# Kernel tuning notes

Measured on AMD Instinct MI355X. Metric: run time of the kernel, lower is better.

The kernel has to match this reference:

```python
import jax, jax.numpy as jnp
import numpy as np

C = 256
CK = C // 8  # query/key projection dim

def conv1x1(x, w, b):
    # x: (B,C,H,W), w: (O,C), b: (O,)
    return jnp.einsum('bchw,oc->bohw', x, w) + b[None, :, None, None]

def conv3x3(x, w, b):
    # w: (O,C,3,3)
    y = jax.lax.conv_general_dilated(x, w, window_strides=(1, 1), padding='SAME',
                                     dimension_numbers=('NCHW', 'OIHW', 'NCHW'))
    return y + b[None, :, None, None]

def setup_inputs() -> dict:
    key = jax.random.key(0)
    ks = jax.random.split(key, 24)
    s = 0.05
    d = {
        'x1': jax.random.normal(ks[0], (4, C, 64, 64), jnp.float32),
        'x2': jax.random.normal(ks[1], (4, C, 64, 64), jnp.float32),
        'wq1': jax.random.normal(ks[2], (CK, C), jnp.float32) * s,
        'bq1': jax.random.normal(ks[3], (CK,), jnp.float32) * s,
        'wk1': jax.random.normal(ks[4], (CK, C), jnp.float32) * s,
        'bk1': jax.random.normal(ks[5], (CK,), jnp.float32) * s,
        'wv1': jax.random.normal(ks[6], (C, C), jnp.float32) * s,
        'bv1': jax.random.normal(ks[7], (C,), jnp.float32) * s,
        'wq2': jax.random.normal(ks[8], (CK, C), jnp.float32) * s,
        'bq2': jax.random.normal(ks[9], (CK,), jnp.float32) * s,
        'wk2': jax.random.normal(ks[10], (CK, C), jnp.float32) * s,
        'bk2': jax.random.normal(ks[11], (CK,), jnp.float32) * s,
        'wv2': jax.random.normal(ks[12], (C, C), jnp.float32) * s,
        'bv2': jax.random.normal(ks[13], (C,), jnp.float32) * s,
        'wd1': jax.random.normal(ks[14], (C, C), jnp.float32) * s,
        'bd1': jax.random.normal(ks[15], (C,), jnp.float32) * s,
        'wd3': jax.random.normal(ks[16], (C, C, 3, 3), jnp.float32) * s,
        'bd3': jax.random.normal(ks[17], (C,), jnp.float32) * s,
        'gamma1': jax.random.normal(ks[18], (1,), jnp.float32) * 0.5,
        'gamma2': jax.random.normal(ks[19], (1,), jnp.float32) * 0.5,
    }
    return d

def reference(x1, x2, wq1, bq1, wk1, bk1, wv1, bv1, wq2, bq2, wk2, bk2, wv2, bv2,
              wd1, bd1, wd3, bd3, gamma1, gamma2):
    B, Cc, H, W = x1.shape
    N = H * W
    # projections (1x1 convs), flattened to (B, d, N)
    q1 = conv1x1(x1, wq1, bq1).reshape(B, CK, N)
    k1 = conv1x1(x1, wk1, bk1).reshape(B, CK, N)
    v1 = conv1x1(x1, wv1, bv1).reshape(B, Cc, N)
    q2 = conv1x1(x2, wq2, bq2).reshape(B, CK, N)
    k2 = conv1x1(x2, wk2, bk2).reshape(B, CK, N)
    v2 = conv1x1(x2, wv2, bv2).reshape(B, Cc, N)
    # cross attention 1: queries from x1, keys/values from x2
    energy1 = jnp.einsum('bdi,bdj->bij', q1, k2)          # (B,N,N)
    attn1 = jax.nn.softmax(energy1, axis=-1)
    out1 = jnp.einsum('bcj,bij->bci', v2, attn1).reshape(B, Cc, H, W)
    # cross attention 2: queries from x2, keys/values from x1
    energy2 = jnp.einsum('bdi,bdj->bij', q2, k1)
    attn2 = jax.nn.softmax(energy2, axis=-1)
    out2 = jnp.einsum('bcj,bij->bci', v1, attn2).reshape(B, Cc, H, W)
    # residual conv branches + gamma-scaled skip (norm1/norm2 in source are dead code)
    out1 = out1 + conv1x1(x1, wd1, bd1) + conv3x3(x1, wd3, bd3)
    out2 = out2 + conv1x1(x2, wd1, bd1) + conv3x3(x2, wd3, bd3)
    out1 = x1 + gamma1[0] * out1
    out2 = x2 + gamma2[0] * out2
    return (out1, out2)
```

## Files before the change

kernel.cpp:

```cpp
#include <hip/hip_runtime.h>
#include <hip/hip_bf16.h>

#define CC 256
#define CKD 32
#define NN 4096
#define HH 64
#define WW 64
#define BB 4

#define LOG2E 1.44269504088896f
#define EXPSHIFT 23.0831203874f

typedef __attribute__((ext_vector_type(8))) short short8;
typedef __attribute__((ext_vector_type(4))) float floatx4;

__device__ __forceinline__ unsigned f2bf(float f) {
  union { float f; unsigned u; } v; v.f = f;
  unsigned r = v.u + 0x7fffu + ((v.u >> 16) & 1u);
  return r >> 16;
}
__device__ __forceinline__ unsigned short f2bf_fast(float f) {
  return (unsigned short)((__float_as_uint(f) + 0x8000u) >> 16);
}
__device__ __forceinline__ float fast_exp2(float x) {
#if __has_builtin(__builtin_amdgcn_exp2f)
  return __builtin_amdgcn_exp2f(x);
#else
  return __expf(x * 0.693147181f);
#endif
}

__global__ __launch_bounds__(256) void xpack_kernel(
    const float* __restrict__ x1, const float* __restrict__ x2,
    unsigned short* __restrict__ Xp) {
  const int t = threadIdx.x;
  const int nb = blockIdx.x, cbk = blockIdx.y, img = blockIdx.z;
  const float* X = ((img >> 2) ? x2 : x1) + (size_t)(img & 3) * CC * NN;
  const int n0 = nb * 64, c0 = cbk * 64;
  __shared__ float tile[64][65];
  const int nl = t & 63, cl0 = t >> 6;
#pragma unroll
  for (int i = 0; i < 16; ++i)
    tile[cl0 + i * 4][nl] = X[(size_t)(c0 + cl0 + i * 4) * NN + n0 + nl];
  __syncthreads();
#pragma unroll
  for (int it = 0; it < 2; ++it) {
    int id = it * 256 + t;
    int nl2 = id >> 3, cc = id & 7;
    short8 v;
#pragma unroll
    for (int j = 0; j < 8; ++j) v[j] = (short)f2bf(tile[cc * 8 + j][nl2]);
    *(short8*)(Xp + (size_t)img * NN * CC + (size_t)(n0 + nl2) * CC + c0 + cc * 8) = v;
  }
}

__global__ __launch_bounds__(256) void wpack_kernel(
    const float* __restrict__ wd1, const float* __restrict__ wd3,
    const float* __restrict__ wq1, const float* __restrict__ wk1,
    const float* __restrict__ wv1,
    const float* __restrict__ wq2, const float* __restrict__ wk2,
    const float* __restrict__ wv2,
    const float* __restrict__ bq1, const float* __restrict__ bk1,
    const float* __restrict__ bv1,
    const float* __restrict__ bq2, const float* __restrict__ bk2,
    const float* __restrict__ bv2,
    unsigned short* __restrict__ Wp, unsigned short* __restrict__ Wqkv,
    float* __restrict__ Bias) {
  const int id = blockIdx.x * 256 + threadIdx.x;
#pragma unroll
  for (int tap = 0; tap < 10; ++tap) {
    float v = (tap < 9) ? wd3[(size_t)id * 9 + tap] : wd1[id];
    Wp[(size_t)tap * (CC * CC) + id] = (unsigned short)f2bf(v);
  }
#pragma unroll
  for (int j = 0; j < 3; ++j) {
    int e = id + j * 65536;
    if (e < 2 * 320 * 256) {
      int inp = e / (320 * 256), rem = e % (320 * 256);
      int o = rem >> 8, c = rem & 255;
      float v;
      if (inp == 0)
        v = (o < 32) ? wq1[o * 256 + c] * LOG2E
            : (o < 64) ? wk1[(o - 32) * 256 + c] : wv1[(o - 64) * 256 + c];
      else
        v = (o < 32) ? wq2[o * 256 + c] * LOG2E
            : (o < 64) ? wk2[(o - 32) * 256 + c] : wv2[(o - 64) * 256 + c];
      Wqkv[e] = (unsigned short)f2bf(v);
    }
  }
  if (id < 640) {
    int inp = id / 320, o = id % 320;
    float v;
    if (inp == 0) v = (o < 32) ? bq1[o] * LOG2E
                      : (o < 64) ? bk1[o - 32] : bv1[o - 64];
    else          v = (o < 32) ? bq2[o] * LOG2E
                      : (o < 64) ? bk2[o - 32] : bv2[o - 64];
    Bias[id] = v;
  }
}

__global__ __launch_bounds__(256) void proj_mfma_kernel(
    const unsigned short* __restrict__ Xp, const unsigned short* __restrict__ Wqkv,
    const float* __restrict__ Bias,
    unsigned short* __restrict__ Qp1, unsigned short* __restrict__ Kp1,
    unsigned short* __restrict__ Vp1,
    unsigned short* __restrict__ Qp2, unsigned short* __restrict__ Kp2,
    unsigned short* __restrict__ Vp2) {
  const int t = threadIdx.x;
  const int w = t >> 6, lane = t & 63;
  const int l15 = lane & 15, g = lane >> 4;
  const int img = blockIdx.x, pb = blockIdx.y;
  const int pix0 = pb * 64;
  const int inp = img >> 2, b = img & 3;
  const unsigned short* Xi = Xp + (size_t)img * NN * CC;
  const unsigned short* Wb = Wqkv + (size_t)inp * 320 * CC;
  const float* Bi = Bias + inp * 320;
  unsigned short* Qp = (inp ? Qp2 : Qp1) + (size_t)b * NN * CKD;
  unsigned short* Kp = (inp ? Kp2 : Kp1) + (size_t)b * NN * CKD;
  unsigned short* Vp = (inp ? Vp2 : Vp1) + (size_t)b * NN * CC;

  __shared__ unsigned short tile[320][72];

  floatx4 acc[4][5];
#pragma unroll
  for (int mf = 0; mf < 4; ++mf)
#pragma unroll
    for (int nf = 0; nf < 5; ++nf) acc[mf][nf] = (floatx4){0.f, 0.f, 0.f, 0.f};
  const int o0w = w * 80;

#pragma unroll
  for (int cb = 0; cb < 8; ++cb) {
    short8 a[4], bfr[5];
#pragma unroll
    for (int mf = 0; mf < 4; ++mf)
      a[mf] = *(const short8*)(Xi + (size_t)(pix0 + mf * 16 + l15) * CC + cb * 32 + g * 8);
#pragma unroll
    for (int nf = 0; nf < 5; ++nf)
      bfr[nf] = *(const short8*)(Wb + (size_t)(o0w + nf * 16 + l15) * CC + cb * 32 + g * 8);
#pragma unroll
    for (int nf = 0; nf < 5; ++nf)
#pragma unroll
      for (int mf = 0; mf < 4; ++mf)
        acc[mf][nf] = __builtin_amdgcn_mfma_f32_16x16x32_bf16(
            a[mf], bfr[nf], acc[mf][nf], 0, 0, 0);
  }

#pragma unroll
  for (int nf = 0; nf < 5; ++nf) {
    float bs = Bi[o0w + nf * 16 + l15];
#pragma unroll
    for (int mf = 0; mf < 4; ++mf) {
      uint2 pk;
      pk.x = f2bf(acc[mf][nf][0] + bs) | (f2bf(acc[mf][nf][1] + bs) << 16);
      pk.y = f2bf(acc[mf][nf][2] + bs) | (f2bf(acc[mf][nf][3] + bs) << 16);
      *(uint2*)&tile[o0w + nf * 16 + l15][mf * 16 + g * 4] = pk;
    }
  }
  __syncthreads();

  {
    const int pix = t >> 2, ch = t & 3;
    short8 vq, vk;
#pragma unroll
    for (int e = 0; e < 8; ++e) {
      vq[e] = (short)tile[ch * 8 + e][pix];
      vk[e] = (short)tile[32 + ch * 8 + e][pix];
    }
    *(short8*)(Qp + (size_t)(pix0 + pix) * CKD + ch * 8) = vq;
    *(short8*)(Kp + (size_t)(pix0 + pix) * CKD + ch * 8) = vk;
  }
#pragma unroll
  for (int it = 0; it < 8; ++it) {
    short8 vv = *(const short8*)&tile[64 + t][it * 8];
    *(short8*)(Vp + ((size_t)((pix0 >> 3) + it) * CC + t) * 8) = vv;
  }
}

__global__ __launch_bounds__(256, 2) void conv_mfma_kernel(
    const unsigned short* __restrict__ Xp, const unsigned short* __restrict__ Wp,
    const float* __restrict__ bd1, const float* __restrict__ bd3,
    unsigned short* __restrict__ R1, unsigned short* __restrict__ R2) {
  const int t = threadIdx.x;
  const int w = t >> 6, lane = t & 63;
  const int l15 = lane & 15, g = lane >> 4;
  const int ob = blockIdx.x, img = blockIdx.y, pb = blockIdx.z;
  const int o0 = ob * 128, n0 = pb * 128, y0 = pb * 2;
  const int wm = w >> 1, wn = w & 1;

  const unsigned short* Xi = Xp + (size_t)img * NN * CC;
  unsigned short* R = ((img >> 2) ? R2 : R1) + (size_t)(img & 3) * CC * NN;

  __shared__ unsigned short xs[4][66][72];

  floatx4 acc[4][4];
#pragma unroll
  for (int m = 0; m < 4; ++m)
#pragma unroll
    for (int n = 0; n < 4; ++n) acc[m][n] = (floatx4){0.f, 0.f, 0.f, 0.f};

  for (int cb = 0; cb < 4; ++cb) {
    const int c0 = cb * 64;
    __syncthreads();
#pragma unroll
    for (int it = 0; it < 9; ++it) {
      int id = it * 256 + t;
      if (id < 2112) {
        int r = id / 528, rem = id % 528;
        int col = rem >> 3, cc = rem & 7;
        int y = y0 - 1 + r, x = col - 1;
        short8 v = {0, 0, 0, 0, 0, 0, 0, 0};
        if (y >= 0 && y < HH && x >= 0 && x < WW)
          v = *(const short8*)(Xi + (size_t)(y * WW + x) * CC + c0 + cc * 8);
        *(short8*)&xs[r][col][cc * 8] = v;
      }
    }
    __syncthreads();
#pragma unroll
    for (int tap = 0; tap < 10; ++tap) {
      const int dy = (tap < 9) ? tap / 3 - 1 : 0;
      const int dx = (tap < 9) ? tap % 3 - 1 : 0;
      const int rrow = 1 + wn + dy;
      const unsigned short* wrow =
          Wp + (size_t)(tap * CC + o0 + wm * 64 + l15) * CC + c0 + g * 8;
#pragma unroll
      for (int ks = 0; ks < 2; ++ks) {
        short8 af[4], bf[4];
#pragma unroll
        for (int m = 0; m < 4; ++m)
          af[m] = *(const short8*)(wrow + (size_t)(m * 16) * CC + ks * 32);
#pragma unroll
        for (int n = 0; n < 4; ++n)
          bf[n] = *(const short8*)&xs[rrow][1 + n * 16 + l15 + dx][ks * 32 + g * 8];
#pragma unroll
        for (int m = 0; m < 4; ++m)
#pragma unroll
          for (int n = 0; n < 4; ++n)
            acc[m][n] = __builtin_amdgcn_mfma_f32_16x16x32_bf16(
                af[m], bf[n], acc[m][n], 0, 0, 0);
      }
    }
  }

#pragma unroll
  for (int m = 0; m < 4; ++m) {
    int ob2 = o0 + wm * 64 + m * 16 + g * 4;
    float bs[4];
#pragma unroll
    for (int r = 0; r < 4; ++r) bs[r] = bd1[ob2 + r] + bd3[ob2 + r];
#pragma unroll
    for (int n = 0; n < 4; ++n) {
      int pix = n0 + wn * 64 + n * 16 + l15;
#pragma unroll
      for (int r = 0; r < 4; ++r)
        R[(size_t)(ob2 + r) * NN + pix] = f2bf_fast(acc[m][n][r] + bs[r]);
    }
  }
}

__global__ __launch_bounds__(256, 2) void attn_kernel(
    const unsigned short* __restrict__ Qp1, const unsigned short* __restrict__ Kp1,
    const unsigned short* __restrict__ Qp2, const unsigned short* __restrict__ Kp2,
    const unsigned short* __restrict__ Vp1, const unsigned short* __restrict__ Vp2,
    const unsigned short* __restrict__ R1, const unsigned short* __restrict__ R2,
    const float* __restrict__ x1, const float* __restrict__ x2,
    const float* __restrict__ g1, const float* __restrict__ g2,
    float* __restrict__ out) {
  const int t = threadIdx.x;
  const int w = t >> 6, lane = t & 63;
  const int l15 = lane & 15, g = lane >> 4;
  const int att = blockIdx.x, b = blockIdx.y;
  const int i0 = blockIdx.z * 64;

  const unsigned short *Qp, *Kp, *Vp, *Rb; const float *x; float gamma; float* o;
  if (att == 0) { Qp = Qp1; Kp = Kp2; Vp = Vp2; Rb = R1; x = x1; gamma = g1[0]; o = out; }
  else          { Qp = Qp2; Kp = Kp1; Vp = Vp1; Rb = R2; x = x2; gamma = g2[0];
                  o = out + (size_t)BB * CC * NN; }
  Qp += (size_t)b * NN * CKD; Kp += (size_t)b * NN * CKD; Vp += (size_t)b * NN * CC;
  Rb += (size_t)b * CC * NN; x += (size_t)b * CC * NN; o += (size_t)b * CC * NN;

  __shared__ unsigned short p_s[2][64][72];
  __shared__ float l_s[64];

  short8 bq = *(const short8*)(Qp + (size_t)(i0 + w * 16 + l15) * CKD + g * 8);

  floatx4 acc[4][4];
#pragma unroll
  for (int a = 0; a < 4; ++a)
#pragma unroll
    for (int c = 0; c < 4; ++c) acc[a][c] = (floatx4){0.f, 0.f, 0.f, 0.f};
  float l_acc = 0.f;
  const floatx4 zinit = {-EXPSHIFT, -EXPSHIFT, -EXPSHIFT, -EXPSHIFT};

  short8 kr[2][4], vr[2][8];
#pragma unroll
  for (int js = 0; js < 4; ++js)
    kr[0][js] = *(const short8*)(Kp + (size_t)(js * 16 + l15) * CKD + g * 8);
#pragma unroll
  for (int ks = 0; ks < 2; ++ks)
#pragma unroll
    for (int cs = 0; cs < 4; ++cs)
      vr[0][ks * 4 + cs] = *(const short8*)(Vp +
          ((size_t)(ks * 4 + g) * CC + (w * 64 + cs * 16 + l15)) * 8);

#pragma unroll 2
  for (int jt = 0; jt < NN / 64; ++jt) {
    const int cur = jt & 1, nxt = cur ^ 1;
    if (jt + 1 < NN / 64) {
      const size_t j0n = (size_t)(jt + 1) * 64;
#pragma unroll
      for (int js = 0; js < 4; ++js)
        kr[nxt][js] = *(const short8*)(Kp + (j0n + js * 16 + l15) * CKD + g * 8);
#pragma unroll
      for (int ks = 0; ks < 2; ++ks)
#pragma unroll
        for (int cs = 0; cs < 4; ++cs)
          vr[nxt][ks * 4 + cs] = *(const short8*)(Vp +
              (((j0n >> 3) + ks * 4 + g) * CC + (w * 64 + cs * 16 + l15)) * 8);
    }
#pragma unroll
    for (int js = 0; js < 4; ++js) {
      floatx4 s = __builtin_amdgcn_mfma_f32_16x16x32_bf16(kr[cur][js], bq, zinit, 0, 0, 0);
      float p0 = fast_exp2(s[0]);
      float p1 = fast_exp2(s[1]);
      float p2 = fast_exp2(s[2]);
      float p3 = fast_exp2(s[3]);
      l_acc += (p0 + p1) + (p2 + p3);
      unsigned u0 = __float_as_uint(p0) + 0x8000u;
      unsigned u1 = __float_as_uint(p1) + 0x8000u;
      unsigned u2 = __float_as_uint(p2) + 0x8000u;
      unsigned u3 = __float_as_uint(p3) + 0x8000u;
      uint2 pk;
      pk.x = __builtin_amdgcn_perm(u1, u0, 0x07060302u);
      pk.y = __builtin_amdgcn_perm(u3, u2, 0x07060302u);
      *(uint2*)&p_s[cur][w * 16 + l15][js * 16 + g * 4] = pk;
    }
    __syncthreads();
#pragma unroll
    for (int ks = 0; ks < 2; ++ks) {
      short8 ap[4];
#pragma unroll
      for (int isub = 0; isub < 4; ++isub)
        ap[isub] = *(const short8*)&p_s[cur][isub * 16 + l15][ks * 32 + g * 8];
#pragma unroll
      for (int cs = 0; cs < 4; ++cs)
#pragma unroll
        for (int isub = 0; isub < 4; ++isub)
          acc[isub][cs] = __builtin_amdgcn_mfma_f32_16x16x32_bf16(
              ap[isub], vr[cur][ks * 4 + cs], acc[isub][cs], 0, 0, 0);
    }
  }

  l_acc += __shfl_xor(l_acc, 16);
  l_acc += __shfl_xor(l_acc, 32);
  if (g == 0) l_s[w * 16 + l15] = l_acc;
  __syncthreads();

#pragma unroll
  for (int isub = 0; isub < 4; ++isub) {
    float linv[4];
#pragma unroll
    for (int r = 0; r < 4; ++r) linv[r] = 1.f / l_s[isub * 16 + g * 4 + r];
#pragma unroll
    for (int cs = 0; cs < 4; ++cs) {
      int c = w * 64 + cs * 16 + l15;
      size_t base = (size_t)c * NN + i0 + isub * 16 + g * 4;
      float4 xr = *(const float4*)(x + base);
      uint2 rr = *(const uint2*)(Rb + base);
      float r0 = __uint_as_float(rr.x << 16);
      float r1 = __uint_as_float(rr.x & 0xffff0000u);
      float r2 = __uint_as_float(rr.y << 16);
      float r3 = __uint_as_float(rr.y & 0xffff0000u);
      float4 ov;
      ov.x = xr.x + gamma * (acc[isub][cs][0] * linv[0] + r0);
      ov.y = xr.y + gamma * (acc[isub][cs][1] * linv[1] + r1);
      ov.z = xr.z + gamma * (acc[isub][cs][2] * linv[2] + r2);
      ov.w = xr.w + gamma * (acc[isub][cs][3] * linv[3] + r3);
      *(float4*)(o + base) = ov;
    }
  }
}

extern "C" void kernel_launch(void* const* d_in, const int* in_sizes, int n_in,
                              void* d_out, int out_size, void* d_ws, size_t ws_size,
                              hipStream_t stream) {
  const float* x1  = (const float*)d_in[0];
  const float* x2  = (const float*)d_in[1];
  const float* wq1 = (const float*)d_in[2];
  const float* bq1 = (const float*)d_in[3];
  const float* wk1 = (const float*)d_in[4];
  const float* bk1 = (const float*)d_in[5];
  const float* wv1 = (const float*)d_in[6];
  const float* bv1 = (const float*)d_in[7];
  const float* wq2 = (const float*)d_in[8];
  const float* bq2 = (const float*)d_in[9];
  const float* wk2 = (const float*)d_in[10];
  const float* bk2 = (const float*)d_in[11];
  const float* wv2 = (const float*)d_in[12];
  const float* bv2 = (const float*)d_in[13];
  const float* wd1 = (const float*)d_in[14];
  const float* bd1 = (const float*)d_in[15];
  const float* wd3 = (const float*)d_in[16];
  const float* bd3 = (const float*)d_in[17];
  const float* g1  = (const float*)d_in[18];
  const float* g2  = (const float*)d_in[19];
  float* out = (float*)d_out;

  const size_t QB = (size_t)BB * NN * CKD * 2;
  const size_t VB = (size_t)BB * NN * CC * 2;
  const size_t RB = (size_t)BB * NN * CC * 2;
  const size_t XB = (size_t)2 * BB * NN * CC * 2;
  const size_t WPB = (size_t)10 * CC * CC * 2;
  const size_t WQB = (size_t)2 * 320 * CC * 2;
  char* base = (char*)d_ws;
  unsigned short* R1 = (unsigned short*)(base);
  unsigned short* R2 = (unsigned short*)(base + RB);
  unsigned short* Qp1 = (unsigned short*)(base + 2 * RB);
  unsigned short* Kp1 = (unsigned short*)(base + 2 * RB + QB);
  unsigned short* Qp2 = (unsigned short*)(base + 2 * RB + 2 * QB);
  unsigned short* Kp2 = (unsigned short*)(base + 2 * RB + 3 * QB);
  unsigned short* Vp1 = (unsigned short*)(base + 2 * RB + 4 * QB);
  unsigned short* Vp2 = (unsigned short*)(base + 2 * RB + 4 * QB + VB);
  unsigned short* Xp  = (unsigned short*)(base + 2 * RB + 4 * QB + 2 * VB);
  unsigned short* Wp  = (unsigned short*)(base + 2 * RB + 4 * QB + 2 * VB + XB);
  unsigned short* Wqkv = (unsigned short*)(base + 2 * RB + 4 * QB + 2 * VB + XB + WPB);
  float* Bias = (float*)(base + 2 * RB + 4 * QB + 2 * VB + XB + WPB + WQB);

  xpack_kernel<<<dim3(NN / 64, CC / 64, 2 * BB), 256, 0, stream>>>(x1, x2, Xp);
  wpack_kernel<<<dim3(CC * CC / 256), 256, 0, stream>>>(
      wd1, wd3, wq1, wk1, wv1, wq2, wk2, wv2,
      bq1, bk1, bv1, bq2, bk2, bv2, Wp, Wqkv, Bias);

  proj_mfma_kernel<<<dim3(2 * BB, NN / 64), 256, 0, stream>>>(
      Xp, Wqkv, Bias, Qp1, Kp1, Vp1, Qp2, Kp2, Vp2);

  conv_mfma_kernel<<<dim3(2, 2 * BB, NN / 128), 256, 0, stream>>>(
      Xp, Wp, bd1, bd3, R1, R2);

  attn_kernel<<<dim3(2, BB, NN / 64), 256, 0, stream>>>(
      Qp1, Kp1, Qp2, Kp2, Vp1, Vp2, R1, R2, x1, x2, g1, g2, out);
}
```

Measured before the change: 316.9 us.

## Fuse input packing into projection, widen conv and attention blocks to 512 threads

The separate xpack kernel is removed. The projection kernel now loads fp32 x, converts it to bf16 in shared memory, writes the packed copy for the conv kernel, and runs its MFMAs from LDS. The conv kernel uses 512 threads over 4 image rows per block. The attention kernel uses 512 threads (8 waves) that split the key tiles and channels, with partial row sums reduced through shared memory and a software-pipelined K/V prefetch across ping-pong P buffers. The aim is to cut one launch and one global round trip and to raise occupancy, at the cost of more registers per wave and more synchronisation.

```diff
diff --git a/kernel.cpp b/kernel.cpp
--- a/kernel.cpp
+++ b/kernel.cpp
@@ -19,8 +19,8 @@
   unsigned r = v.u + 0x7fffu + ((v.u >> 16) & 1u);
   return r >> 16;
 }
-__device__ __forceinline__ unsigned short f2bf_fast(float f) {
-  return (unsigned short)((__float_as_uint(f) + 0x8000u) >> 16);
+__device__ __forceinline__ unsigned f2bf_fast(float f) {
+  return (__float_as_uint(f) + 0x8000u) >> 16;
 }
 __device__ __forceinline__ float fast_exp2(float x) {
 #if __has_builtin(__builtin_amdgcn_exp2f)
@@ -29,30 +29,8 @@
   return __expf(x * 0.693147181f);
 #endif
 }
-
-__global__ __launch_bounds__(256) void xpack_kernel(
-    const float* __restrict__ x1, const float* __restrict__ x2,
-    unsigned short* __restrict__ Xp) {
-  const int t = threadIdx.x;
-  const int nb = blockIdx.x, cbk = blockIdx.y, img = blockIdx.z;
-  const float* X = ((img >> 2) ? x2 : x1) + (size_t)(img & 3) * CC * NN;
-  const int n0 = nb * 64, c0 = cbk * 64;
-  __shared__ float tile[64][65];
-  const int nl = t & 63, cl0 = t >> 6;
-#pragma unroll
-  for (int i = 0; i < 16; ++i)
-    tile[cl0 + i * 4][nl] = X[(size_t)(c0 + cl0 + i * 4) * NN + n0 + nl];
-  __syncthreads();
-#pragma unroll
-  for (int it = 0; it < 2; ++it) {
-    int id = it * 256 + t;
-    int nl2 = id >> 3, cc = id & 7;
-    short8 v;
-#pragma unroll
-    for (int j = 0; j < 8; ++j) v[j] = (short)f2bf(tile[cc * 8 + j][nl2]);
-    *(short8*)(Xp + (size_t)img * NN * CC + (size_t)(n0 + nl2) * CC + c0 + cc * 8) = v;
-  }
-}
+__device__ __forceinline__ float bf_lo(unsigned u) { return __uint_as_float(u << 16); }
+__device__ __forceinline__ float bf_hi(unsigned u) { return __uint_as_float(u & 0xffff0000u); }
 
 __global__ __launch_bounds__(256) void wpack_kernel(
     const float* __restrict__ wd1, const float* __restrict__ wd3,
@@ -99,9 +77,10 @@
   }
 }
 
-__global__ __launch_bounds__(256) void proj_mfma_kernel(
-    const unsigned short* __restrict__ Xp, const unsigned short* __restrict__ Wqkv,
-    const float* __restrict__ Bias,
+__global__ __launch_bounds__(256) void proj_kernel(
+    const float* __restrict__ x1, const float* __restrict__ x2,
+    const unsigned short* __restrict__ Wqkv, const float* __restrict__ Bias,
+    unsigned short* __restrict__ Xp,
     unsigned short* __restrict__ Qp1, unsigned short* __restrict__ Kp1,
     unsigned short* __restrict__ Vp1,
     unsigned short* __restrict__ Qp2, unsigned short* __restrict__ Kp2,
@@ -112,14 +91,40 @@
   const int img = blockIdx.x, pb = blockIdx.y;
   const int pix0 = pb * 64;
   const int inp = img >> 2, b = img & 3;
-  const unsigned short* Xi = Xp + (size_t)img * NN * CC;
+  const float* X = (inp ? x2 : x1) + (size_t)b * CC * NN;
   const unsigned short* Wb = Wqkv + (size_t)inp * 320 * CC;
   const float* Bi = Bias + inp * 320;
   unsigned short* Qp = (inp ? Qp2 : Qp1) + (size_t)b * NN * CKD;
   unsigned short* Kp = (inp ? Kp2 : Kp1) + (size_t)b * NN * CKD;
   unsigned short* Vp = (inp ? Vp2 : Vp1) + (size_t)b * NN * CC;
-
-  __shared__ unsigned short tile[320][72];
+  unsigned short* Xo = Xp + (size_t)img * NN * CC;
+
+  __shared__ union {
+    float ftile[64][65];
+    unsigned short otile[320][72];
+  } pu;
+  __shared__ unsigned short xt[64][264];
+
+  const int nl = t & 63, cl0 = t >> 6;
+  for (int cb = 0; cb < 4; ++cb) {
+    const int c0 = cb * 64;
+    if (cb) __syncthreads();
+#pragma unroll
+    for (int i = 0; i < 16; ++i)
+      pu.ftile[cl0 + i * 4][nl] = X[(size_t)(c0 + cl0 + i * 4) * NN + pix0 + nl];
+    __syncthreads();
+#pragma unroll
+    for (int it = 0; it < 2; ++it) {
+      int id = it * 256 + t;
+      int p = id >> 3, cc = id & 7;
+      short8 v;
+#pragma unroll
+      for (int j = 0; j < 8; ++j) v[j] = (short)f2bf(pu.ftile[cc * 8 + j][p]);
+      *(short8*)&xt[p][c0 + cc * 8] = v;
+      *(short8*)(Xo + (size_t)(pix0 + p) * CC + c0 + cc * 8) = v;
+    }
+  }
+  __syncthreads();
 
   floatx4 acc[4][5];
 #pragma unroll
@@ -133,7 +138,7 @@
     short8 a[4], bfr[5];
 #pragma unroll
     for (int mf = 0; mf < 4; ++mf)
-      a[mf] = *(const short8*)(Xi + (size_t)(pix0 + mf * 16 + l15) * CC + cb * 32 + g * 8);
+      a[mf] = *(const short8*)&xt[mf * 16 + l15][cb * 32 + g * 8];
 #pragma unroll
     for (int nf = 0; nf < 5; ++nf)
       bfr[nf] = *(const short8*)(Wb + (size_t)(o0w + nf * 16 + l15) * CC + cb * 32 + g * 8);
@@ -153,7 +158,7 @@
       uint2 pk;
       pk.x = f2bf(acc[mf][nf][0] + bs) | (f2bf(acc[mf][nf][1] + bs) << 16);
       pk.y = f2bf(acc[mf][nf][2] + bs) | (f2bf(acc[mf][nf][3] + bs) << 16);
-      *(uint2*)&tile[o0w + nf * 16 + l15][mf * 16 + g * 4] = pk;
+      *(uint2*)&pu.otile[o0w + nf * 16 + l15][mf * 16 + g * 4] = pk;
     }
   }
   __syncthreads();
@@ -163,20 +168,20 @@
     short8 vq, vk;
 #pragma unroll
     for (int e = 0; e < 8; ++e) {
-      vq[e] = (short)tile[ch * 8 + e][pix];
-      vk[e] = (short)tile[32 + ch * 8 + e][pix];
+      vq[e] = (short)pu.otile[ch * 8 + e][pix];
+      vk[e] = (short)pu.otile[32 + ch * 8 + e][pix];
     }
     *(short8*)(Qp + (size_t)(pix0 + pix) * CKD + ch * 8) = vq;
     *(short8*)(Kp + (size_t)(pix0 + pix) * CKD + ch * 8) = vk;
   }
 #pragma unroll
   for (int it = 0; it < 8; ++it) {
-    short8 vv = *(const short8*)&tile[64 + t][it * 8];
+    short8 vv = *(const short8*)&pu.otile[64 + t][it * 8];
     *(short8*)(Vp + ((size_t)((pix0 >> 3) + it) * CC + t) * 8) = vv;
   }
 }
 
-__global__ __launch_bounds__(256, 2) void conv_mfma_kernel(
+__global__ __launch_bounds__(512, 4) void conv_kernel(
     const unsigned short* __restrict__ Xp, const unsigned short* __restrict__ Wp,
     const float* __restrict__ bd1, const float* __restrict__ bd3,
     unsigned short* __restrict__ R1, unsigned short* __restrict__ R2) {
@@ -184,33 +189,33 @@
   const int w = t >> 6, lane = t & 63;
   const int l15 = lane & 15, g = lane >> 4;
   const int ob = blockIdx.x, img = blockIdx.y, pb = blockIdx.z;
-  const int o0 = ob * 128, n0 = pb * 128, y0 = pb * 2;
-  const int wm = w >> 1, wn = w & 1;
+  const int o0 = ob * 128, y0 = pb * 4;
+  const int wm = w >> 2, wp = w & 3;
 
   const unsigned short* Xi = Xp + (size_t)img * NN * CC;
   unsigned short* R = ((img >> 2) ? R2 : R1) + (size_t)(img & 3) * CC * NN;
 
-  __shared__ unsigned short xs[4][66][72];
-
-  floatx4 acc[4][4];
+  __shared__ unsigned short xs[6][66][72];
+
+  floatx4 ac[4][4];
 #pragma unroll
   for (int m = 0; m < 4; ++m)
 #pragma unroll
-    for (int n = 0; n < 4; ++n) acc[m][n] = (floatx4){0.f, 0.f, 0.f, 0.f};
+    for (int n = 0; n < 4; ++n) ac[m][n] = (floatx4){0.f, 0.f, 0.f, 0.f};
 
   for (int cb = 0; cb < 4; ++cb) {
     const int c0 = cb * 64;
-    __syncthreads();
-#pragma unroll
-    for (int it = 0; it < 9; ++it) {
-      int id = it * 256 + t;
-      if (id < 2112) {
+    if (cb) __syncthreads();
+#pragma unroll
+    for (int it = 0; it < 7; ++it) {
+      int id = it * 512 + t;
+      if (id < 3168) {
         int r = id / 528, rem = id % 528;
         int col = rem >> 3, cc = rem & 7;
-        int y = y0 - 1 + r, x = col - 1;
+        int y = y0 - 1 + r, xx = col - 1;
         short8 v = {0, 0, 0, 0, 0, 0, 0, 0};
-        if (y >= 0 && y < HH && x >= 0 && x < WW)
-          v = *(const short8*)(Xi + (size_t)(y * WW + x) * CC + c0 + cc * 8);
+        if (y >= 0 && y < HH && xx >= 0 && xx < WW)
+          v = *(const short8*)(Xi + (size_t)(y * WW + xx) * CC + c0 + cc * 8);
         *(short8*)&xs[r][col][cc * 8] = v;
       }
     }
@@ -219,9 +224,9 @@
     for (int tap = 0; tap < 10; ++tap) {
       const int dy = (tap < 9) ? tap / 3 - 1 : 0;
       const int dx = (tap < 9) ? tap % 3 - 1 : 0;
-      const int rrow = 1 + wn + dy;
+      const int rrow = 1 + wp + dy;
       const unsigned short* wrow =
-          Wp + (size_t)(tap * CC + o0 + wm * 64 + l15) * CC + c0 + g * 8;
+          Wp + ((size_t)tap * CC + o0 + wm * 64 + l15) * CC + c0 + g * 8;
 #pragma unroll
       for (int ks = 0; ks < 2; ++ks) {
         short8 af[4], bf[4];
@@ -235,8 +240,8 @@
         for (int m = 0; m < 4; ++m)
 #pragma unroll
           for (int n = 0; n < 4; ++n)
-            acc[m][n] = __builtin_amdgcn_mfma_f32_16x16x32_bf16(
-                af[m], bf[n], acc[m][n], 0, 0, 0);
+            ac[m][n] = __builtin_amdgcn_mfma_f32_16x16x32_bf16(
+                af[m], bf[n], ac[m][n], 0, 0, 0);
       }
     }
   }
@@ -249,15 +254,15 @@
     for (int r = 0; r < 4; ++r) bs[r] = bd1[ob2 + r] + bd3[ob2 + r];
 #pragma unroll
     for (int n = 0; n < 4; ++n) {
-      int pix = n0 + wn * 64 + n * 16 + l15;
+      int pix = (y0 + wp) * WW + n * 16 + l15;
 #pragma unroll
       for (int r = 0; r < 4; ++r)
-        R[(size_t)(ob2 + r) * NN + pix] = f2bf_fast(acc[m][n][r] + bs[r]);
-    }
-  }
-}
-
-__global__ __launch_bounds__(256, 2) void attn_kernel(
+        R[(size_t)(ob2 + r) * NN + pix] = (unsigned short)f2bf_fast(ac[m][n][r] + bs[r]);
+    }
+  }
+}
+
+__global__ __launch_bounds__(512, 4) void attn_kernel(
     const unsigned short* __restrict__ Qp1, const unsigned short* __restrict__ Kp1,
     const unsigned short* __restrict__ Qp2, const unsigned short* __restrict__ Kp2,
     const unsigned short* __restrict__ Vp1, const unsigned short* __restrict__ Vp2,
@@ -270,6 +275,9 @@
   const int l15 = lane & 15, g = lane >> 4;
   const int att = blockIdx.x, b = blockIdx.y;
   const int i0 = blockIdx.z * 64;
+  const int jof = (w & 3) * 16;
+  const int ih32 = (w >> 2) * 32;
+  const int c0w = w * 32;
 
   const unsigned short *Qp, *Kp, *Vp, *Rb; const float *x; float gamma; float* o;
   if (att == 0) { Qp = Qp1; Kp = Kp2; Vp = Vp2; Rb = R1; x = x1; gamma = g1[0]; o = out; }
@@ -279,102 +287,112 @@
   Rb += (size_t)b * CC * NN; x += (size_t)b * CC * NN; o += (size_t)b * CC * NN;
 
   __shared__ unsigned short p_s[2][64][72];
-  __shared__ float l_s[64];
-
-  short8 bq = *(const short8*)(Qp + (size_t)(i0 + w * 16 + l15) * CKD + g * 8);
-
-  floatx4 acc[4][4];
-#pragma unroll
-  for (int a = 0; a < 4; ++a)
-#pragma unroll
-    for (int c = 0; c < 4; ++c) acc[a][c] = (floatx4){0.f, 0.f, 0.f, 0.f};
-  float l_acc = 0.f;
+  __shared__ float l_part[4][64];
+
+  short8 bq0 = *(const short8*)(Qp + (size_t)(i0 + ih32 + l15) * CKD + g * 8);
+  short8 bq1 = *(const short8*)(Qp + (size_t)(i0 + ih32 + 16 + l15) * CKD + g * 8);
+
+  floatx4 acc[4][2];
+#pragma unroll
+  for (int m = 0; m < 4; ++m)
+#pragma unroll
+    for (int cs = 0; cs < 2; ++cs) acc[m][cs] = (floatx4){0.f, 0.f, 0.f, 0.f};
+  float l0 = 0.f, l1 = 0.f;
   const floatx4 zinit = {-EXPSHIFT, -EXPSHIFT, -EXPSHIFT, -EXPSHIFT};
 
-  short8 kr[2][4], vr[2][8];
-#pragma unroll
-  for (int js = 0; js < 4; ++js)
-    kr[0][js] = *(const short8*)(Kp + (size_t)(js * 16 + l15) * CKD + g * 8);
-#pragma unroll
-  for (int ks = 0; ks < 2; ++ks)
-#pragma unroll
-    for (int cs = 0; cs < 4; ++cs)
-      vr[0][ks * 4 + cs] = *(const short8*)(Vp +
-          ((size_t)(ks * 4 + g) * CC + (w * 64 + cs * 16 + l15)) * 8);
-
-#pragma unroll 2
-  for (int jt = 0; jt < NN / 64; ++jt) {
-    const int cur = jt & 1, nxt = cur ^ 1;
-    if (jt + 1 < NN / 64) {
-      const size_t j0n = (size_t)(jt + 1) * 64;
-#pragma unroll
-      for (int js = 0; js < 4; ++js)
-        kr[nxt][js] = *(const short8*)(Kp + (j0n + js * 16 + l15) * CKD + g * 8);
-#pragma unroll
-      for (int ks = 0; ks < 2; ++ks)
-#pragma unroll
-        for (int cs = 0; cs < 4; ++cs)
-          vr[nxt][ks * 4 + cs] = *(const short8*)(Vp +
-              (((j0n >> 3) + ks * 4 + g) * CC + (w * 64 + cs * 16 + l15)) * 8);
-    }
-#pragma unroll
-    for (int js = 0; js < 4; ++js) {
-      floatx4 s = __builtin_amdgcn_mfma_f32_16x16x32_bf16(kr[cur][js], bq, zinit, 0, 0, 0);
-      float p0 = fast_exp2(s[0]);
-      float p1 = fast_exp2(s[1]);
-      float p2 = fast_exp2(s[2]);
-      float p3 = fast_exp2(s[3]);
-      l_acc += (p0 + p1) + (p2 + p3);
-      unsigned u0 = __float_as_uint(p0) + 0x8000u;
-      unsigned u1 = __float_as_uint(p1) + 0x8000u;
-      unsigned u2 = __float_as_uint(p2) + 0x8000u;
-      unsigned u3 = __float_as_uint(p3) + 0x8000u;
-      uint2 pk;
-      pk.x = __builtin_amdgcn_perm(u1, u0, 0x07060302u);
-      pk.y = __builtin_amdgcn_perm(u3, u2, 0x07060302u);
-      *(uint2*)&p_s[cur][w * 16 + l15][js * 16 + g * 4] = pk;
-    }
-    __syncthreads();
+  short8 kr0, kr1, vr[4];
+  auto LOADK = [&](int tt, short8& d) {
+    d = *(const short8*)(Kp + ((size_t)tt * 64 + jof + l15) * CKD + g * 8);
+  };
+  auto LOADV = [&](int tt) {
+#pragma unroll
+    for (int ks = 0; ks < 2; ++ks)
+#pragma unroll
+      for (int cs = 0; cs < 2; ++cs)
+        vr[ks * 2 + cs] = *(const short8*)(Vp +
+            (((size_t)tt * 8 + ks * 4 + g) * CC + (c0w + cs * 16 + l15)) * 8);
+  };
+  auto GEMM1 = [&](const short8& kf, unsigned short (*ps)[72]) {
+    floatx4 s0 = __builtin_amdgcn_mfma_f32_16x16x32_bf16(kf, bq0, zinit, 0, 0, 0);
+    floatx4 s1 = __builtin_amdgcn_mfma_f32_16x16x32_bf16(kf, bq1, zinit, 0, 0, 0);
+    float p00 = fast_exp2(s0[0]), p01 = fast_exp2(s0[1]);
+    float p02 = fast_exp2(s0[2]), p03 = fast_exp2(s0[3]);
+    float p10 = fast_exp2(s1[0]), p11 = fast_exp2(s1[1]);
+    float p12 = fast_exp2(s1[2]), p13 = fast_exp2(s1[3]);
+    l0 += (p00 + p01) + (p02 + p03);
+    l1 += (p10 + p11) + (p12 + p13);
+    uint2 pk0, pk1;
+    pk0.x = __builtin_amdgcn_perm(__float_as_uint(p01) + 0x8000u,
+                                  __float_as_uint(p00) + 0x8000u, 0x07060302u);
+    pk0.y = __builtin_amdgcn_perm(__float_as_uint(p03) + 0x8000u,
+                                  __float_as_uint(p02) + 0x8000u, 0x07060302u);
+    pk1.x = __builtin_amdgcn_perm(__float_as_uint(p11) + 0x8000u,
+                                  __float_as_uint(p10) + 0x8000u, 0x07060302u);
+    pk1.y = __builtin_amdgcn_perm(__float_as_uint(p13) + 0x8000u,
+                                  __float_as_uint(p12) + 0x8000u, 0x07060302u);
+    *(uint2*)&ps[ih32 + l15][jof + g * 4] = pk0;
+    *(uint2*)&ps[ih32 + 16 + l15][jof + g * 4] = pk1;
+  };
+  auto GEMM2 = [&](unsigned short (*ps)[72]) {
 #pragma unroll
     for (int ks = 0; ks < 2; ++ks) {
       short8 ap[4];
 #pragma unroll
-      for (int isub = 0; isub < 4; ++isub)
-        ap[isub] = *(const short8*)&p_s[cur][isub * 16 + l15][ks * 32 + g * 8];
-#pragma unroll
-      for (int cs = 0; cs < 4; ++cs)
-#pragma unroll
-        for (int isub = 0; isub < 4; ++isub)
-          acc[isub][cs] = __builtin_amdgcn_mfma_f32_16x16x32_bf16(
-              ap[isub], vr[cur][ks * 4 + cs], acc[isub][cs], 0, 0, 0);
-    }
-  }
-
-  l_acc += __shfl_xor(l_acc, 16);
-  l_acc += __shfl_xor(l_acc, 32);
-  if (g == 0) l_s[w * 16 + l15] = l_acc;
+      for (int m = 0; m < 4; ++m)
+        ap[m] = *(const short8*)&ps[m * 16 + l15][ks * 32 + g * 8];
+#pragma unroll
+      for (int cs = 0; cs < 2; ++cs)
+#pragma unroll
+        for (int m = 0; m < 4; ++m)
+          acc[m][cs] = __builtin_amdgcn_mfma_f32_16x16x32_bf16(
+              ap[m], vr[ks * 2 + cs], acc[m][cs], 0, 0, 0);
+    }
+  };
+
+  LOADK(0, kr0); LOADK(1, kr1);
+  GEMM1(kr0, p_s[0]);
   __syncthreads();
 
-#pragma unroll
-  for (int isub = 0; isub < 4; ++isub) {
+  for (int jt = 0; jt < 64; jt += 2) {
+    LOADV(jt);
+    if (jt + 2 < 64) LOADK(jt + 2, kr0);
+    GEMM1(kr1, p_s[1]);
+    GEMM2(p_s[0]);
+    __syncthreads();
+    LOADV(jt + 1);
+    if (jt + 3 < 64) LOADK(jt + 3, kr1);
+    if (jt + 2 < 64) GEMM1(kr0, p_s[0]);
+    GEMM2(p_s[1]);
+    __syncthreads();
+  }
+
+  l0 += __shfl_xor(l0, 16); l0 += __shfl_xor(l0, 32);
+  l1 += __shfl_xor(l1, 16); l1 += __shfl_xor(l1, 32);
+  if (g == 0) {
+    l_part[w & 3][ih32 + l15] = l0;
+    l_part[w & 3][ih32 + 16 + l15] = l1;
+  }
+  __syncthreads();
+
+#pragma unroll
+  for (int m = 0; m < 4; ++m) {
     float linv[4];
 #pragma unroll
-    for (int r = 0; r < 4; ++r) linv[r] = 1.f / l_s[isub * 16 + g * 4 + r];
-#pragma unroll
-    for (int cs = 0; cs < 4; ++cs) {
-      int c = w * 64 + cs * 16 + l15;
-      size_t base = (size_t)c * NN + i0 + isub * 16 + g * 4;
+    for (int r = 0; r < 4; ++r) {
+      int il = m * 16 + g * 4 + r;
+      linv[r] = 1.f / (l_part[0][il] + l_part[1][il] + l_part[2][il] + l_part[3][il]);
+    }
+#pragma unroll
+    for (int cs = 0; cs < 2; ++cs) {
+      int c = c0w + cs * 16 + l15;
+      size_t base = (size_t)c * NN + i0 + m * 16 + g * 4;
       float4 xr = *(const float4*)(x + base);
       uint2 rr = *(const uint2*)(Rb + base);
-      float r0 = __uint_as_float(rr.x << 16);
-      float r1 = __uint_as_float(rr.x & 0xffff0000u);
-      float r2 = __uint_as_float(rr.y << 16);
-      float r3 = __uint_as_float(rr.y & 0xffff0000u);
       float4 ov;
-      ov.x = xr.x + gamma * (acc[isub][cs][0] * linv[0] + r0);
-      ov.y = xr.y + gamma * (acc[isub][cs][1] * linv[1] + r1);
-      ov.z = xr.z + gamma * (acc[isub][cs][2] * linv[2] + r2);
-      ov.w = xr.w + gamma * (acc[isub][cs][3] * linv[3] + r3);
+      ov.x = xr.x + gamma * (acc[m][cs][0] * linv[0] + bf_lo(rr.x));
+      ov.y = xr.y + gamma * (acc[m][cs][1] * linv[1] + bf_hi(rr.x));
+      ov.z = xr.z + gamma * (acc[m][cs][2] * linv[2] + bf_lo(rr.y));
+      ov.w = xr.w + gamma * (acc[m][cs][3] * linv[3] + bf_hi(rr.y));
       *(float4*)(o + base) = ov;
     }
   }
@@ -425,17 +443,16 @@
   unsigned short* Wqkv = (unsigned short*)(base + 2 * RB + 4 * QB + 2 * VB + XB + WPB);
   float* Bias = (float*)(base + 2 * RB + 4 * QB + 2 * VB + XB + WPB + WQB);
 
-  xpack_kernel<<<dim3(NN / 64, CC / 64, 2 * BB), 256, 0, stream>>>(x1, x2, Xp);
   wpack_kernel<<<dim3(CC * CC / 256), 256, 0, stream>>>(
       wd1, wd3, wq1, wk1, wv1, wq2, wk2, wv2,
       bq1, bk1, bv1, bq2, bk2, bv2, Wp, Wqkv, Bias);
 
-  proj_mfma_kernel<<<dim3(2 * BB, NN / 64), 256, 0, stream>>>(
-      Xp, Wqkv, Bias, Qp1, Kp1, Vp1, Qp2, Kp2, Vp2);
-
-  conv_mfma_kernel<<<dim3(2, 2 * BB, NN / 128), 256, 0, stream>>>(
+  proj_kernel<<<dim3(2 * BB, NN / 64), 256, 0, stream>>>(
+      x1, x2, Wqkv, Bias, Xp, Qp1, Kp1, Vp1, Qp2, Kp2, Vp2);
+
+  conv_kernel<<<dim3(2, 2 * BB, HH / 4), 512, 0, stream>>>(
       Xp, Wp, bd1, bd3, R1, R2);
 
-  attn_kernel<<<dim3(2, BB, NN / 64), 256, 0, stream>>>(
+  attn_kernel<<<dim3(2, BB, NN / 64), 512, 0, stream>>>(
       Qp1, Kp1, Qp2, Kp2, Vp1, Vp2, R1, R2, x1, x2, g1, g2, out);
 }
```

Result: slower. 331.0 us (+4.5%).
